# Optimization experiments

Hardware: AMD Instinct MI355X
Metric: run time of the kernel (lower is better)

The kernel has to match this reference:

```python
import jax, jax.numpy as jnp
import numpy as np

C_S = 384; C_Z = 128; C_RES = 128; H = 12; HD = 32; L = 8; RB = 2; NA = 7
TSF = 10.0; EPS = 1e-8; B = 2; N = 512; NRES = 21


def layernorm(x, g, b, eps=1e-5):
    m = jnp.mean(x, -1, keepdims=True)
    v = jnp.mean((x - m) ** 2, -1, keepdims=True)
    return (x - m) * jax.lax.rsqrt(v + eps) * g + b


def lin(x, w, b=None):
    y = x @ w.T
    return y if b is None else y + b


def rot_vec(R, v):
    return jnp.einsum('...ij,...j->...i', R, v)


def make_rigid(n, ca, c, eps=1e-7):
    # Gram-Schmidt backbone frame construction (openfold make_transform_from_reference)
    t = -ca
    n_xyz = n + t; c_xyz = c + t
    cx, cy, cz = c_xyz[..., 0], c_xyz[..., 1], c_xyz[..., 2]
    z = jnp.zeros_like(cx); o = jnp.ones_like(cx)
    nrm = jnp.sqrt(eps + cx**2 + cy**2)
    s1 = -cy / nrm; c1 = cx / nrm
    R1 = jnp.stack([jnp.stack([c1, -s1, z], -1), jnp.stack([s1, c1, z], -1), jnp.stack([z, z, o], -1)], -2)
    nrm2 = jnp.sqrt(eps + cx**2 + cy**2 + cz**2)
    s2 = cz / nrm2; c2 = jnp.sqrt(cx**2 + cy**2) / nrm2
    R2 = jnp.stack([jnp.stack([c2, z, s2], -1), jnp.stack([z, o, z], -1), jnp.stack([-s2, z, c2], -1)], -2)
    Rc = R2 @ R1
    n2 = rot_vec(Rc, n_xyz)
    ny, nz = n2[..., 1], n2[..., 2]
    nrm3 = jnp.sqrt(eps + ny**2 + nz**2)
    sn = -nz / nrm3; cn = ny / nrm3
    Rn = jnp.stack([jnp.stack([o, z, z], -1), jnp.stack([z, cn, -sn], -1), jnp.stack([z, sn, cn], -1)], -2)
    R = jnp.swapaxes(Rn @ Rc, -1, -2)
    return R, ca


def to4x4(R, t):
    bot = jnp.zeros(R.shape[:-2] + (1, 4), R.dtype).at[..., 0, 3].set(1.0)
    top = jnp.concatenate([R, t[..., None]], -1)
    return jnp.concatenate([top, bot], -2)


def compose(R1, t1, R2, t2):
    return R1 @ R2, rot_vec(R1, t2) + t1


def structure_fwd(s, z, aatype, mask, ln_s_g, ln_s_b, ln_z_g, ln_z_b, w_in, b_in, w_b, b_b,
                  attn_ln_g, attn_ln_b, attn_wqkv, attn_wo, attn_bo, attn_wg, attn_bg,
                  tr_ln_g, tr_ln_b, tr_w1, tr_b1, tr_w2, tr_b2, w_bb, b_bb,
                  ar_win, ar_bin, ar_winit, ar_binit, ar_w1, ar_b1, ar_w2, ar_b2, ar_wout, ar_bout,
                  default_frames, group_idx, atom_mask, lit_positions):
    Bd, Nd = s.shape[:2]
    s = layernorm(s, ln_s_g, ln_s_b)
    s_init = s
    s = lin(s, w_in, b_in)
    zn = layernorm(z, ln_z_g, ln_z_b)
    bmat = lin(zn, w_b, b_b)                                # [B,N,N,L*H]
    bmat = jnp.transpose(bmat, (0, 3, 1, 2)).reshape(Bd, L, H, Nd, Nd)
    key_mask = (mask[:, None, None, :] == 0)
    for i in range(L):
        xn = layernorm(s, attn_ln_g[i], attn_ln_b[i])
        t = lin(xn, attn_wqkv[i]).reshape(Bd, Nd, H, 3 * HD).transpose(0, 2, 1, 3)
        q, k, v = jnp.split(t, 3, axis=-1)                  # each [B,H,N,HD]
        a = jnp.einsum('bhqc,bhkc->bhqk', q * HD ** -0.5, k) + bmat[:, i]
        a = jnp.where(key_mask, -1e9, a)
        a = jax.nn.softmax(a, axis=-1)
        y = jnp.einsum('bhqk,bhkc->bqhc', a, v).reshape(Bd, Nd, C_S)
        g = jax.nn.sigmoid(lin(xn, attn_wg[i], attn_bg[i]))
        s = s + lin(g * y, attn_wo[i], attn_bo[i])
        xt = layernorm(s, tr_ln_g[i], tr_ln_b[i])
        s = s + lin(jax.nn.relu(lin(xt, tr_w1[i], tr_b1[i])), tr_w2[i], tr_b2[i])
    # angle resnet
    a0 = lin(jax.nn.relu(s_init), ar_winit, ar_binit)
    a = lin(jax.nn.relu(s), ar_win, ar_bin) + a0
    for j in range(RB):
        h = lin(jax.nn.relu(a), ar_w1[j], ar_b1[j])
        h = lin(jax.nn.relu(h), ar_w2[j], ar_b2[j])
        a = a + h
    ang = lin(jax.nn.relu(a), ar_wout, ar_bout).reshape(Bd, Nd, NA, 2)
    unnorm = ang
    denom = jnp.sqrt(jnp.maximum(jnp.sum(ang ** 2, -1, keepdims=True), EPS))
    angles = ang / denom
    # backbone rigid from predicted pseudo-atoms
    n_, ca_, c_ = jnp.split(lin(s, w_bb, b_bb), 3, axis=-1)
    Rbb, tbb = make_rigid(n_, ca_, c_)
    tbb = tbb * TSF
    # torsion_angles_to_frames
    d4 = default_frames[aatype]                             # [B,N,8,4,4]
    dR = d4[..., :3, :3]; dt = d4[..., :3, 3]
    bb_sin = jnp.zeros(angles.shape[:-2] + (1,), angles.dtype)
    bb_cos = jnp.ones_like(bb_sin)
    sin_a = jnp.concatenate([bb_sin, angles[..., 0]], -1)   # [B,N,8]
    cos_a = jnp.concatenate([bb_cos, angles[..., 1]], -1)
    z8 = jnp.zeros_like(sin_a); o8 = jnp.ones_like(sin_a)
    Ra = jnp.stack([jnp.stack([o8, z8, z8], -1), jnp.stack([z8, cos_a, -sin_a], -1), jnp.stack([z8, sin_a, cos_a], -1)], -2)
    Rf = dR @ Ra; tf = dt
    R5, t5 = compose(Rf[..., 4, :, :], tf[..., 4, :], Rf[..., 5, :, :], tf[..., 5, :])
    R6, t6 = compose(R5, t5, Rf[..., 6, :, :], tf[..., 6, :])
    R7, t7 = compose(R6, t6, Rf[..., 7, :, :], tf[..., 7, :])
    Rall = jnp.concatenate([Rf[..., :5, :, :], jnp.stack([R5, R6, R7], -3)], -3)
    tall = jnp.concatenate([tf[..., :5, :], jnp.stack([t5, t6, t7], -2)], -2)
    Rg = jnp.einsum('bnij,bngjk->bngik', Rbb, Rall)
    tg = jnp.einsum('bnij,bngj->bngi', Rbb, tall) + tbb[..., None, :]
    # frames + literature positions -> atom14
    oh = jax.nn.one_hot(group_idx[aatype], 8, dtype=Rg.dtype)   # [B,N,14,8]
    Ratom = jnp.einsum('bnag,bngij->bnaij', oh, Rg)
    tatom = jnp.einsum('bnag,bngi->bnai', oh, tg)
    lit = lit_positions[aatype]                             # [B,N,14,3]
    pred = jnp.einsum('bnaij,bnaj->bnai', Ratom, lit) + tatom
    pred = pred * atom_mask[aatype][..., None]
    return angles, unnorm, to4x4(Rbb, tbb), to4x4(Rg, tg), pred, s


def setup_inputs():
    key = jax.random.key(0)
    ks = iter(jax.random.split(key, 64))
    nrm = lambda shape: jax.random.normal(next(ks), shape, jnp.float32) * 0.02
    d = {}
    d['s'] = jax.random.normal(next(ks), (B, N, C_S), jnp.float32)
    d['z'] = jax.random.normal(next(ks), (B, N, N, C_Z), jnp.float32)
    d['aatype'] = jax.random.randint(next(ks), (B, N), 0, NRES)
    d['mask'] = jax.random.randint(next(ks), (B, N), 0, 2).astype(jnp.int32)
    d['ln_s_g'] = jnp.ones(C_S); d['ln_s_b'] = jnp.zeros(C_S)
    d['ln_z_g'] = jnp.ones(C_Z); d['ln_z_b'] = jnp.zeros(C_Z)
    d['w_in'] = nrm((C_S, C_S)); d['b_in'] = jnp.zeros(C_S)
    d['w_b'] = nrm((L * H, C_Z)); d['b_b'] = jnp.zeros(L * H)
    d['attn_ln_g'] = jnp.ones((L, C_S)); d['attn_ln_b'] = jnp.zeros((L, C_S))
    d['attn_wqkv'] = nrm((L, 3 * C_S, C_S))
    d['attn_wo'] = nrm((L, C_S, C_S)); d['attn_bo'] = jnp.zeros((L, C_S))
    d['attn_wg'] = nrm((L, C_S, C_S)); d['attn_bg'] = jnp.ones((L, C_S))
    d['tr_ln_g'] = jnp.ones((L, C_S)); d['tr_ln_b'] = jnp.zeros((L, C_S))
    d['tr_w1'] = nrm((L, C_S, C_S)); d['tr_b1'] = jnp.zeros((L, C_S))
    d['tr_w2'] = nrm((L, C_S, C_S)); d['tr_b2'] = jnp.zeros((L, C_S))
    d['w_bb'] = nrm((9, C_S)); d['b_bb'] = jnp.zeros(9)
    d['ar_win'] = nrm((C_RES, C_S)); d['ar_bin'] = jnp.zeros(C_RES)
    d['ar_winit'] = nrm((C_RES, C_S)); d['ar_binit'] = jnp.zeros(C_RES)
    d['ar_w1'] = nrm((RB, C_RES, C_RES)); d['ar_b1'] = jnp.zeros((RB, C_RES))
    d['ar_w2'] = nrm((RB, C_RES, C_RES)); d['ar_b2'] = jnp.zeros((RB, C_RES))
    d['ar_wout'] = nrm((2 * NA, C_RES)); d['ar_bout'] = jnp.zeros(2 * NA)
    df = jnp.tile(jnp.eye(4, dtype=jnp.float32), (NRES, 8, 1, 1))
    df = df.at[..., :3, 3].set(jax.random.normal(next(ks), (NRES, 8, 3)))
    d['default_frames'] = df
    d['group_idx'] = jax.random.randint(next(ks), (NRES, 14), 0, 8)
    d['atom_mask'] = (jax.random.uniform(next(ks), (NRES, 14)) < 0.9).astype(jnp.float32)
    d['lit_positions'] = jax.random.normal(next(ks), (NRES, 14, 3), jnp.float32)
    return d


def reference(s, z, aatype, mask, ln_s_g, ln_s_b, ln_z_g, ln_z_b, w_in, b_in, w_b, b_b,
              attn_ln_g, attn_ln_b, attn_wqkv, attn_wo, attn_bo, attn_wg, attn_bg,
              tr_ln_g, tr_ln_b, tr_w1, tr_b1, tr_w2, tr_b2, w_bb, b_bb,
              ar_win, ar_bin, ar_winit, ar_binit, ar_w1, ar_b1, ar_w2, ar_b2, ar_wout, ar_bout,
              default_frames, group_idx, atom_mask, lit_positions):
    return structure_fwd(s, z, aatype, mask, ln_s_g, ln_s_b, ln_z_g, ln_z_b, w_in, b_in, w_b, b_b,
                         attn_ln_g, attn_ln_b, attn_wqkv, attn_wo, attn_bo, attn_wg, attn_bg,
                         tr_ln_g, tr_ln_b, tr_w1, tr_b1, tr_w2, tr_b2, w_bb, b_bb,
                         ar_win, ar_bin, ar_winit, ar_binit, ar_w1, ar_b1, ar_w2, ar_b2, ar_wout, ar_bout,
                         default_frames, group_idx, atom_mask, lit_positions)
```

## Files before the change

### kernel.cpp

```cpp
#include <hip/hip_runtime.h>
#include <hip/hip_bf16.h>

typedef __attribute__((ext_vector_type(8))) short bf16x8;
typedef __attribute__((ext_vector_type(4))) float f32x4;
typedef unsigned short u16;

__device__ __forceinline__ u16 f2bf(float f) {
  union { __hip_bfloat16 b; u16 u; } v;
  v.b = __float2bfloat16(f);
  return v.u;
}
__device__ __forceinline__ float bf2f(u16 s) {
  union { unsigned u; float f; } v; v.u = ((unsigned)s) << 16;
  return v.f;
}
__device__ __forceinline__ f32x4 mfma_bf16(bf16x8 a, bf16x8 b, f32x4 c) {
  return __builtin_amdgcn_mfma_f32_16x16x32_bf16(a, b, c, 0, 0, 0);
}
__device__ __forceinline__ void split2(float x, u16& h, u16& l) {
  h = f2bf(x);
  l = f2bf(x - bf2f(h));
}
template <int SPL>
__device__ __forceinline__ void splitN(float x, u16* o) {
// ... 30 lines not shown
}
struct P3 { const float* s; u16* d; int n; };
struct Prep3Args { P3 j[4]; };
__global__ __launch_bounds__(256) void prep3_kernel(Prep3Args A, int total4) {
  for (int i4 = blockIdx.x * 256 + threadIdx.x; i4 < total4; i4 += gridDim.x * 256) {
    int i = i4 * 4;
    #pragma unroll
    for (int jj = 0; jj < 4; jj++) {
      if (i < A.j[jj].n) {
        const float* src = A.j[jj].s;
        u16* d0 = A.j[jj].d;
        u16* d1 = d0 + A.j[jj].n;
        u16* d2 = d1 + A.j[jj].n;
        float4 v = *(const float4*)(src + i);
        float xv[4] = {v.x, v.y, v.z, v.w};
        ushort4 o0, o1, o2;
        u16* po0 = (u16*)&o0; u16* po1 = (u16*)&o1; u16* po2 = (u16*)&o2;
        #pragma unroll
        for (int e = 0; e < 4; e++) {
          u16 tmp[3]; splitN<3>(xv[e], tmp);
          po0[e] = tmp[0]; po1[e] = tmp[1]; po2[e] = tmp[2];
        }
        *(ushort4*)(d0 + i) = o0;
        *(ushort4*)(d1 + i) = o1;
        *(ushort4*)(d2 + i) = o2;
        break;
      }
      i -= A.j[jj].n;
    }
  }
}

__global__ __launch_bounds__(256) void ln_kernel(
    const float* __restrict__ x, const float* __restrict__ gamma,
    const float* __restrict__ beta, float* __restrict__ o, int rows, int C) {
  int wid = threadIdx.x >> 6, lane = threadIdx.x & 63;
  int row = blockIdx.x * 4 + wid;
  if (row >= rows) return;
  const float* xr = x + (size_t)row * C;
  float s = 0.f, s2 = 0.f;
  for (int c = lane; c < C; c += 64) { float v = xr[c]; s += v; s2 += v * v; }
  #pragma unroll
  for (int off = 32; off >= 1; off >>= 1) {
    s += __shfl_xor(s, off);
    s2 += __shfl_xor(s2, off);
  }
  float m = s / C;
  float var = s2 / C - m * m;
  float rs = rsqrtf(var + 1e-5f);
  float* orow = o + (size_t)row * C;
  for (int c = lane; c < C; c += 64) orow[c] = (xr[c] - m) * rs * gamma[c] + beta[c];
}

template <int SPL, int LNA, int INRELU, int ACT, int ACC, int STATS, int OUT2>
__global__ __launch_bounds__(128) void gemm_kernel(
    const float* __restrict__ A, const float* __restrict__ pin,
    const float* __restrict__ lng, const float* __restrict__ lnb,
    const u16* __restrict__ w0p, const u16* __restrict__ w1p, const u16* __restrict__ w2p,
    const float* __restrict__ bias,
    float* __restrict__ O, float* __restrict__ O2, float* __restrict__ pout,
    int M, int N, int K) {
  __shared__ __align__(16) u16 a_pl[SPL][16][72];
  __shared__ __align__(16) u16 w_pl[SPL][64][72];
  const int n0 = blockIdx.x * 64, m0 = blockIdx.y * 16;
  const int t = threadIdx.x;
  const int wid = t >> 6, lane = t & 63;
  const int cl = lane & 15, cg = lane >> 4;
  const int ar = t >> 3, aq = t & 7;
  const int wr = t >> 1, wh2 = t & 1;
  const float* ap = A + (size_t)(m0 + ar) * K + aq * 8;
  const u16* wp[3] = {nullptr, nullptr, nullptr};
  {
    const u16* tmp[3] = {w0p, w1p, w2p};
    #pragma unroll
    for (int p = 0; p < SPL; p++) wp[p] = tmp[p] + (size_t)(n0 + wr) * K + wh2 * 32;
  }
  float rm = 0.f, rrs = 1.f;
  if (LNA) {
    float s = 0.f, s2 = 0.f;
    #pragma unroll
    for (int pq = 0; pq < 12; pq++) {
      s  += pin[(m0 + ar) * 32 + pq * 2];
      s2 += pin[(m0 + ar) * 32 + pq * 2 + 1];
    }
    rm = s * (1.f / 384.f);
    rrs = rsqrtf(s2 * (1.f / 384.f) - rm * rm + 1e-5f);
  }
  float4 ra[2], rg[2], rb4[2];
  uint4 rw[SPL][4];
  auto GLOAD = [&](int k0) {
    ra[0] = ((const float4*)(ap + k0))[0];
    ra[1] = ((const float4*)(ap + k0))[1];
    #pragma unroll
    for (int p = 0; p < SPL; p++)
      #pragma unroll
      for (int e = 0; e < 4; e++) rw[p][e] = *(const uint4*)(wp[p] + k0 + e * 8);
    if (LNA) {
      rg[0]  = ((const float4*)(lng + k0 + aq * 8))[0];
      rg[1]  = ((const float4*)(lng + k0 + aq * 8))[1];
      rb4[0] = ((const float4*)(lnb + k0 + aq * 8))[0];
      rb4[1] = ((const float4*)(lnb + k0 + aq * 8))[1];
    }
  };
  GLOAD(0);
  f32x4 acc[2] = {};
  for (int k0 = 0; k0 < K; k0 += 64) {
    {
      float av[8] = {ra[0].x, ra[0].y, ra[0].z, ra[0].w, ra[1].x, ra[1].y, ra[1].z, ra[1].w};
      if (LNA) {
        float gv[8] = {rg[0].x, rg[0].y, rg[0].z, rg[0].w, rg[1].x, rg[1].y, rg[1].z, rg[1].w};
        float bv[8] = {rb4[0].x, rb4[0].y, rb4[0].z, rb4[0].w, rb4[1].x, rb4[1].y, rb4[1].z, rb4[1].w};
        #pragma unroll
        for (int j = 0; j < 8; j++) av[j] = (av[j] - rm) * rrs * gv[j] + bv[j];
      }
      if (INRELU) {
        #pragma unroll
        for (int j = 0; j < 8; j++) av[j] = fmaxf(av[j], 0.f);
      }
      u16 sh[SPL][8];
      #pragma unroll
      for (int j = 0; j < 8; j++) {
        u16 tmp[SPL]; splitN<SPL>(av[j], tmp);
        #pragma unroll
        for (int p = 0; p < SPL; p++) sh[p][j] = tmp[p];
      }
      #pragma unroll
      for (int p = 0; p < SPL; p++) {
        *(uint4*)&a_pl[p][ar][aq * 8] = *(const uint4*)&sh[p][0];
        #pragma unroll
        for (int e = 0; e < 4; e++) *(uint4*)&w_pl[p][wr][wh2 * 32 + e * 8] = rw[p][e];
      }
    }
    __syncthreads();
    if (k0 + 64 < K) GLOAD(k0 + 64);
    #pragma unroll
    for (int ks2 = 0; ks2 < 2; ks2++) {
      bf16x8 av_[SPL];
      #pragma unroll
      for (int p = 0; p < SPL; p++)
        av_[p] = *(const bf16x8*)&a_pl[p][cl][ks2 * 32 + cg * 8];
      bf16x8 bv[SPL][2];
      #pragma unroll
      for (int p = 0; p < SPL; p++)
        #pragma unroll
        for (int ntl = 0; ntl < 2; ntl++)
          bv[p][ntl] = *(const bf16x8*)&w_pl[p][(wid * 2 + ntl) * 16 + cl][ks2 * 32 + cg * 8];
      #pragma unroll
      for (int d = 0; d < SPL; d++)
        #pragma unroll
        for (int i2 = 0; i2 <= d; i2++) {
          #pragma unroll
          for (int ntl = 0; ntl < 2; ntl++)
            acc[ntl] = mfma_bf16(av_[i2], bv[d - i2][ntl], acc[ntl]);
        }
    }
    __syncthreads();
  }
  float ps[4], ps2[4];
  #pragma unroll
  for (int i = 0; i < 4; i++) { ps[i] = 0.f; ps2[i] = 0.f; }
  #pragma unroll
  for (int ntl = 0; ntl < 2; ntl++) {
    #pragma unroll
    for (int i = 0; i < 4; i++) {
      int r = m0 + cg * 4 + i;
      int c = n0 + (wid * 2 + ntl) * 16 + cl;
      float v = acc[ntl][i];
      if (bias) v += bias[c];
      if (ACT == 1) v = fmaxf(v, 0.f);
      if (ACT == 2) v = 1.f / (1.f + __expf(-v));
      size_t oi = (size_t)r * N + c;
      float nv = ACC ? (O[oi] + v) : v;
      O[oi] = nv;
      if (OUT2) O2[oi] = nv;
      if (STATS) { ps[i] += nv; ps2[i] += nv * nv; }
    }
  }
  if (STATS) {
    #pragma unroll
    for (int i = 0; i < 4; i++) {
      #pragma unroll
      for (int off = 1; off < 16; off <<= 1) {
        ps[i] += __shfl_xor(ps[i], off);
        ps2[i] += __shfl_xor(ps2[i], off);
      }
    }
    if (cl == 0) {
      #pragma unroll
      for (int i = 0; i < 4; i++) {
        int r = m0 + cg * 4 + i;
        pout[r * 32 + (blockIdx.x * 2 + wid) * 2] = ps[i];
        pout[r * 32 + (blockIdx.x * 2 + wid) * 2 + 1] = ps2[i];
      }
    }
  }
}

__global__ __launch_bounds__(128) void gemm_qkvg_kernel(
    const float* __restrict__ A, const float* __restrict__ pin,
    const float* __restrict__ lng, const float* __restrict__ lnb,
    const u16* __restrict__ wqh, const u16* __restrict__ wql,
    const u16* __restrict__ wgh, const u16* __restrict__ wgl,
    const float* __restrict__ bg,
    u16* __restrict__ qkvh, u16* __restrict__ qkvl, float* __restrict__ gbuf) {
  __shared__ __align__(16) u16 a_pl[2][16][72];
  __shared__ __align__(16) u16 w_pl[2][64][72];
  const int n0 = blockIdx.x * 64, m0 = blockIdx.y * 16;
  const bool isg = (n0 >= 1152);
  const int t = threadIdx.x;
  const int wid = t >> 6, lane = t & 63;
  const int cl = lane & 15, cg = lane >> 4;
  const int ar = t >> 3, aq = t & 7;
  const int wr = t >> 1, wh2 = t & 1;
  const float* ap = A + (size_t)(m0 + ar) * 384 + aq * 8;
  const u16* wph = (isg ? wgh + (size_t)(n0 - 1152 + wr) * 384 : wqh + (size_t)(n0 + wr) * 384) + wh2 * 32;
  const u16* wpl = (isg ? wgl + (size_t)(n0 - 1152 + wr) * 384 : wql + (size_t)(n0 + wr) * 384) + wh2 * 32;
  float s = 0.f, s2 = 0.f;
  #pragma unroll
  for (int pq = 0; pq < 12; pq++) {
    s  += pin[(m0 + ar) * 32 + pq * 2];
    s2 += pin[(m0 + ar) * 32 + pq * 2 + 1];
  }
  const float rm = s * (1.f / 384.f);
  const float rrs = rsqrtf(s2 * (1.f / 384.f) - rm * rm + 1e-5f);
  float4 ra[2], rg[2], rb4[2];
  uint4 rwh[4], rwl[4];
  auto GLOAD = [&](int k0) {
    ra[0] = ((const float4*)(ap + k0))[0];
    ra[1] = ((const float4*)(ap + k0))[1];
    #pragma unroll
    for (int e = 0; e < 4; e++) {
      rwh[e] = *(const uint4*)(wph + k0 + e * 8);
      rwl[e] = *(const uint4*)(wpl + k0 + e * 8);
    }
    rg[0]  = ((const float4*)(lng + k0 + aq * 8))[0];
    rg[1]  = ((const float4*)(lng + k0 + aq * 8))[1];
    rb4[0] = ((const float4*)(lnb + k0 + aq * 8))[0];
    rb4[1] = ((const float4*)(lnb + k0 + aq * 8))[1];
  };
  GLOAD(0);
  f32x4 acc[2] = {};
  for (int k0 = 0; k0 < 384; k0 += 64) {
    {
      float av[8] = {ra[0].x, ra[0].y, ra[0].z, ra[0].w, ra[1].x, ra[1].y, ra[1].z, ra[1].w};
      float gv[8] = {rg[0].x, rg[0].y, rg[0].z, rg[0].w, rg[1].x, rg[1].y, rg[1].z, rg[1].w};
      float bv[8] = {rb4[0].x, rb4[0].y, rb4[0].z, rb4[0].w, rb4[1].x, rb4[1].y, rb4[1].z, rb4[1].w};
      u16 sh[2][8];
      #pragma unroll
      for (int j = 0; j < 8; j++) {
        float x = (av[j] - rm) * rrs * gv[j] + bv[j];
        split2(x, sh[0][j], sh[1][j]);
      }
      #pragma unroll
      for (int p = 0; p < 2; p++) *(uint4*)&a_pl[p][ar][aq * 8] = *(const uint4*)&sh[p][0];
      #pragma unroll
      for (int e = 0; e < 4; e++) {
        *(uint4*)&w_pl[0][wr][wh2 * 32 + e * 8] = rwh[e];
        *(uint4*)&w_pl[1][wr][wh2 * 32 + e * 8] = rwl[e];
      }
    }
    __syncthreads();
    if (k0 + 64 < 384) GLOAD(k0 + 64);
    #pragma unroll
    for (int ks2 = 0; ks2 < 2; ks2++) {
      bf16x8 ah = *(const bf16x8*)&a_pl[0][cl][ks2 * 32 + cg * 8];
      bf16x8 al = *(const bf16x8*)&a_pl[1][cl][ks2 * 32 + cg * 8];
      bf16x8 bh[2], bl[2];
      #pragma unroll
      for (int ntl = 0; ntl < 2; ntl++) {
        bh[ntl] = *(const bf16x8*)&w_pl[0][(wid * 2 + ntl) * 16 + cl][ks2 * 32 + cg * 8];
        bl[ntl] = *(const bf16x8*)&w_pl[1][(wid * 2 + ntl) * 16 + cl][ks2 * 32 + cg * 8];
      }
      #pragma unroll
      for (int ntl = 0; ntl < 2; ntl++) {
        acc[ntl] = mfma_bf16(ah, bh[ntl], acc[ntl]);
        acc[ntl] = mfma_bf16(ah, bl[ntl], acc[ntl]);
        acc[ntl] = mfma_bf16(al, bh[ntl], acc[ntl]);
      }
    }
    __syncthreads();
  }
  #pragma unroll
  for (int ntl = 0; ntl < 2; ntl++) {
    #pragma unroll
    for (int i = 0; i < 4; i++) {
      int r = m0 + cg * 4 + i;
      int c = n0 + (wid * 2 + ntl) * 16 + cl;
      float v = acc[ntl][i];
      if (isg) {
        int cc = c - 1152;
        v = 1.f / (1.f + __expf(-(v + bg[cc])));
        gbuf[(size_t)r * 384 + cc] = v;
      } else {
        u16 hh, ll; split2(v, hh, ll);
        qkvh[(size_t)r * 1152 + c] = hh;
        qkvl[(size_t)r * 1152 + c] = ll;
      }
    }
  }
}

__global__ __launch_bounds__(512) void zbmat_kernel(
    const float* __restrict__ z, const float* __restrict__ gamma,
    const float* __restrict__ beta, const u16* __restrict__ wbh,
    const u16* __restrict__ wbl, const float* __restrict__ bbias,
    float* __restrict__ bm) {
  __shared__ __align__(16) u16 w_h[96][136], w_l[96][136];
  __shared__ __align__(16) u16 a_h[2][64][136], a_l[2][64][136];
  const int b = blockIdx.x >> 9, i = blockIdx.x & 511;
  const int t = threadIdx.x;
  for (int idx = t; idx < 1536; idx += 512) {
    int r2 = idx >> 4, c2 = (idx & 15) * 8;
    *(uint4*)&w_h[r2][c2] = *(const uint4*)(wbh + r2 * 128 + c2);
    *(uint4*)&w_l[r2][c2] = *(const uint4*)(wbl + r2 * 128 + c2);
  }
  const int r = t >> 3, q = t & 7;
  const int cq = q * 16;
  const float* zbase = z + ((size_t)(b * 512 + i) * 512) * 128 + (size_t)r * 128 + cq;
  float4 gv[4], bv[4];
  #pragma unroll
  for (int ii = 0; ii < 4; ii++) {
    gv[ii] = *(const float4*)(gamma + cq + ii * 4);
    bv[ii] = *(const float4*)(beta + cq + ii * 4);
  }
  const int wid = t >> 6, lane = t & 63;
  const int cl = lane & 15, cg = lane >> 4;
  const int m = wid & 3, g = wid >> 2;
  const int arow = m * 16 + cl;
  float bb[3];
  #pragma unroll
  for (int nt = 0; nt < 3; nt++) bb[nt] = bbias[(g * 3 + nt) * 16 + cl];
  float4 v[4];

  auto ln_store = [&](int dst) {
    float s = 0.f, s2 = 0.f;
    #pragma unroll
    for (int ii = 0; ii < 4; ii++) {
      s += v[ii].x + v[ii].y + v[ii].z + v[ii].w;
      s2 += v[ii].x * v[ii].x + v[ii].y * v[ii].y + v[ii].z * v[ii].z + v[ii].w * v[ii].w;
    }
    s += __shfl_xor(s, 1); s2 += __shfl_xor(s2, 1);
    s += __shfl_xor(s, 2); s2 += __shfl_xor(s2, 2);
    s += __shfl_xor(s, 4); s2 += __shfl_xor(s2, 4);
    const float mu = s * (1.f / 128.f);
    const float var = s2 * (1.f / 128.f) - mu * mu;
    const float rs = rsqrtf(var + 1e-5f);
    float xv[16];
    #pragma unroll
    for (int w2 = 0; w2 < 4; w2++) {
      float4 x = v[w2], g2 = gv[w2], be = bv[w2];
// ... 375 lines not shown
  const float* lit_pos   = (const float*)d_in[40];

  char* p = (char*)d_ws;
  float* bmat   = (float*)p;          p += 201326592;
  float* s_init = (float*)p;          p += 1572864;
  float* s_cur  = (float*)p;          p += 1572864;
  u16*   qkvh   = (u16*)p;            p += 2359296;
  u16*   qkvl   = (u16*)p;            p += 2359296;
  float* gbuf   = (float*)p;          p += 1572864;
  float* ybuf   = (float*)p;          p += 1572864;
  float* h1buf  = (float*)p;          p += 1572864;
  float* abuf   = (float*)p;          p += 524288;
  float* htmp   = (float*)p;          p += 524288;
  float* pbuf   = (float*)p;          p += 131072;
  float* bbbuf  = (float*)p;          p += 65536;
  float* angraw = (float*)p;          p += 57344;
  u16* ps_qkvw  = (u16*)p;            p += 14155776;
  u16* ps_wg    = (u16*)p;            p += 4718592;
  u16* ps_wo    = (u16*)p;            p += 4718592;
  u16* ps_tr1   = (u16*)p;            p += 4718592;
  u16* ps_tr2   = (u16*)p;            p += 4718592;
  u16* ps_win   = (u16*)p;            p += 589824;
  u16* ps_wb    = (u16*)p;            p += 49152;
  u16* ps_arwin = (u16*)p;            p += 294912;
  u16* ps_arwinit = (u16*)p;          p += 294912;
  u16* ps_arw1  = (u16*)p;            p += 196608;
  u16* ps_arw2  = (u16*)p;            p += 196608;

  float* out    = (float*)d_out;
  float* o_ang  = out;
  float* o_un   = out + 14336;
  float* o_bb4  = out + 28672;
  float* o_rg4  = out + 45056;
  float* o_pred = out + 176128;
  float* o_s    = out + 219136;

  Prep2Args p2;
  p2.j[0] = {attn_wqkv, ps_qkvw, 3538944};
  p2.j[1] = {attn_wg,   ps_wg,   1179648};
  p2.j[2] = {attn_wo,   ps_wo,   1179648};
  p2.j[3] = {tr_w1,     ps_tr1,  1179648};
  p2.j[4] = {tr_w2,     ps_tr2,  1179648};
  p2.j[5] = {w_in,      ps_win,  147456};
  p2.j[6] = {w_b,       ps_wb,   12288};
  prep2_kernel<<<2048, 256, 0, stream>>>(p2, 2104320);
  Prep3Args p3;
  p3.j[0] = {ar_win,   ps_arwin,   49152};
  p3.j[1] = {ar_winit, ps_arwinit, 49152};
  p3.j[2] = {ar_w1,    ps_arw1,    32768};
  p3.j[3] = {ar_w2,    ps_arw2,    32768};
  prep3_kernel<<<160, 256, 0, stream>>>(p3, 40960);

  ln_kernel<<<256, 256, 0, stream>>>(s_in, ln_s_g, ln_s_b, s_init, 1024, 384);
  gemm_kernel<2, 0, 0, 0, 0, 1, 0><<<dim3(6, 64), 128, 0, stream>>>(
      s_init, nullptr, nullptr, nullptr, ps_win, ps_win + 147456, nullptr,
      b_in, s_cur, nullptr, pbuf, 1024, 384, 384);
  zbmat_kernel<<<1024, 512, 0, stream>>>(z_in, ln_z_g, ln_z_b, ps_wb, ps_wb + 12288, b_b, bmat);

  for (int l = 0; l < 8; ++l) {
    gemm_qkvg_kernel<<<dim3(24, 64), 128, 0, stream>>>(
        s_cur, pbuf, attn_ln_g + l * 384, attn_ln_b + l * 384,
        ps_qkvw + (size_t)l * 442368, ps_qkvw + 3538944 + (size_t)l * 442368,
        ps_wg + (size_t)l * 147456, ps_wg + 1179648 + (size_t)l * 147456,
        attn_bg + l * 384, qkvh, qkvl, gbuf);
    attn_kernel<<<384, 128, 0, stream>>>(qkvh, qkvl, bmat, maskp, gbuf, ybuf, l);
    gemm_kernel<2, 0, 0, 0, 1, 1, 0><<<dim3(6, 64), 128, 0, stream>>>(
        ybuf, nullptr, nullptr, nullptr,
        ps_wo + (size_t)l * 147456, ps_wo + 1179648 + (size_t)l * 147456, nullptr,
        attn_bo + l * 384, s_cur, nullptr, pbuf, 1024, 384, 384);
    gemm_kernel<2, 1, 0, 1, 0, 0, 0><<<dim3(6, 64), 128, 0, stream>>>(
        s_cur, pbuf, tr_ln_g + l * 384, tr_ln_b + l * 384,
        ps_tr1 + (size_t)l * 147456, ps_tr1 + 1179648 + (size_t)l * 147456, nullptr,
        tr_b1 + l * 384, h1buf, nullptr, nullptr, 1024, 384, 384);
    if (l < 7)
      gemm_kernel<2, 0, 0, 0, 1, 1, 0><<<dim3(6, 64), 128, 0, stream>>>(
          h1buf, nullptr, nullptr, nullptr,
          ps_tr2 + (size_t)l * 147456, ps_tr2 + 1179648 + (size_t)l * 147456, nullptr,
          tr_b2 + l * 384, s_cur, nullptr, pbuf, 1024, 384, 384);
    else
      gemm_kernel<2, 0, 0, 0, 1, 1, 1><<<dim3(6, 64), 128, 0, stream>>>(
          h1buf, nullptr, nullptr, nullptr,
          ps_tr2 + (size_t)l * 147456, ps_tr2 + 1179648 + (size_t)l * 147456, nullptr,
          tr_b2 + l * 384, s_cur, o_s, pbuf, 1024, 384, 384);
  }

  gemm_kernel<3, 0, 1, 0, 0, 0, 0><<<dim3(2, 64), 128, 0, stream>>>(
      s_cur, nullptr, nullptr, nullptr,
      ps_arwin, ps_arwin + 49152, ps_arwin + 98304,
      ar_bin, abuf, nullptr, nullptr, 1024, 128, 384);
  gemm_kernel<3, 0, 1, 0, 1, 0, 0><<<dim3(2, 64), 128, 0, stream>>>(
      s_init, nullptr, nullptr, nullptr,
      ps_arwinit, ps_arwinit + 49152, ps_arwinit + 98304,
      ar_binit, abuf, nullptr, nullptr, 1024, 128, 384);
  for (int j = 0; j < 2; ++j) {
    gemm_kernel<3, 0, 1, 0, 0, 0, 0><<<dim3(2, 64), 128, 0, stream>>>(
        abuf, nullptr, nullptr, nullptr,
        ps_arw1 + j * 16384, ps_arw1 + 32768 + j * 16384, ps_arw1 + 65536 + j * 16384,
        ar_b1 + j * 128, htmp, nullptr, nullptr, 1024, 128, 128);
    gemm_kernel<3, 0, 1, 0, 1, 0, 0><<<dim3(2, 64), 128, 0, stream>>>(
        htmp, nullptr, nullptr, nullptr,
        ps_arw2 + j * 16384, ps_arw2 + 32768 + j * 16384, ps_arw2 + 65536 + j * 16384,
        ar_b2 + j * 128, abuf, nullptr, nullptr, 1024, 128, 128);
  }

  proj_kernel<9, 384, 0><<<256, 256, 0, stream>>>(s_cur, w_bb, b_bb, bbbuf);
  proj_kernel<14, 128, 1><<<256, 256, 0, stream>>>(abuf, ar_wout, ar_bout, angraw);
  tail_kernel<<<4, 256, 0, stream>>>(angraw, bbbuf, aatype, def_frames, group_idx,
                                     atom_mask, lit_pos, o_ang, o_un, o_bb4, o_rg4, o_pred);
}
```

Before: 1.369 ms.

## Keep full-K weight tiles resident in LDS across multiple M tiles in GEMMs

The 384-wide GEMMs now load the whole 64x384 hi/lo weight slab and the LayerNorm gamma/beta into LDS once per block. Each block then loops over several 16-row M tiles, prefetching the next A rows while it computes, so weights are reused instead of reloaded by many small blocks. The angle-resnet GEMMs move to a 32-row tile variant so each weight load serves twice as many rows. The cost is much larger LDS use per block (about 130KB), which lowers occupancy, and far fewer blocks in the grid.

```diff
diff --git a/kernel.cpp b/kernel.cpp
--- a/kernel.cpp
+++ b/kernel.cpp
@@ -106,250 +106,336 @@
   for (int c = lane; c < C; c += 64) orow[c] = (xr[c] - m) * rs * gamma[c] + beta[c];
 }
 
-template <int SPL, int LNA, int INRELU, int ACT, int ACC, int STATS, int OUT2>
-__global__ __launch_bounds__(128) void gemm_kernel(
+template <int LNA, int ACT, int ACC, int STATS, int OUT2>
+__global__ __launch_bounds__(128) void gemm_ml_kernel(
     const float* __restrict__ A, const float* __restrict__ pin,
     const float* __restrict__ lng, const float* __restrict__ lnb,
-    const u16* __restrict__ w0p, const u16* __restrict__ w1p, const u16* __restrict__ w2p,
+    const u16* __restrict__ wh_, const u16* __restrict__ wl_,
     const float* __restrict__ bias,
     float* __restrict__ O, float* __restrict__ O2, float* __restrict__ pout,
-    int M, int N, int K) {
-  __shared__ __align__(16) u16 a_pl[SPL][16][72];
-  __shared__ __align__(16) u16 w_pl[SPL][64][72];
-  const int n0 = blockIdx.x * 64, m0 = blockIdx.y * 16;
+    int N, int MT) {
+  __shared__ __align__(16) u16 w_pl[2][64][392];
+  __shared__ __align__(16) u16 a_pl[2][16][392];
+  __shared__ float gbs[2][384];
+  const int n0 = blockIdx.x * 64;
+  const int m0g = blockIdx.y * (MT << 4);
   const int t = threadIdx.x;
   const int wid = t >> 6, lane = t & 63;
   const int cl = lane & 15, cg = lane >> 4;
-  const int ar = t >> 3, aq = t & 7;
-  const int wr = t >> 1, wh2 = t & 1;
-  const float* ap = A + (size_t)(m0 + ar) * K + aq * 8;
-  const u16* wp[3] = {nullptr, nullptr, nullptr};
   {
-    const u16* tmp[3] = {w0p, w1p, w2p};
-    #pragma unroll
-    for (int p = 0; p < SPL; p++) wp[p] = tmp[p] + (size_t)(n0 + wr) * K + wh2 * 32;
-  }
-  float rm = 0.f, rrs = 1.f;
-  if (LNA) {
-    float s = 0.f, s2 = 0.f;
-    #pragma unroll
-    for (int pq = 0; pq < 12; pq++) {
-      s  += pin[(m0 + ar) * 32 + pq * 2];
-      s2 += pin[(m0 + ar) * 32 + pq * 2 + 1];
-    }
-    rm = s * (1.f / 384.f);
-    rrs = rsqrtf(s2 * (1.f / 384.f) - rm * rm + 1e-5f);
-  }
-  float4 ra[2], rg[2], rb4[2];
-  uint4 rw[SPL][4];
-  auto GLOAD = [&](int k0) {
-    ra[0] = ((const float4*)(ap + k0))[0];
-    ra[1] = ((const float4*)(ap + k0))[1];
-    #pragma unroll
-    for (int p = 0; p < SPL; p++)
-      #pragma unroll
-      for (int e = 0; e < 4; e++) rw[p][e] = *(const uint4*)(wp[p] + k0 + e * 8);
+    const u16* s0 = wh_ + (size_t)n0 * 384;
+    const u16* s1 = wl_ + (size_t)n0 * 384;
+    for (int idx = t; idx < 3072; idx += 128) {
+      int r = idx / 48, c8 = (idx % 48) * 8;
+      *(uint4*)&w_pl[0][r][c8] = *(const uint4*)(s0 + (size_t)r * 384 + c8);
+      *(uint4*)&w_pl[1][r][c8] = *(const uint4*)(s1 + (size_t)r * 384 + c8);
+    }
     if (LNA) {
-      rg[0]  = ((const float4*)(lng + k0 + aq * 8))[0];
-      rg[1]  = ((const float4*)(lng + k0 + aq * 8))[1];
-      rb4[0] = ((const float4*)(lnb + k0 + aq * 8))[0];
-      rb4[1] = ((const float4*)(lnb + k0 + aq * 8))[1];
-    }
-  };
-  GLOAD(0);
-  f32x4 acc[2] = {};
-  for (int k0 = 0; k0 < K; k0 += 64) {
-    {
-      float av[8] = {ra[0].x, ra[0].y, ra[0].z, ra[0].w, ra[1].x, ra[1].y, ra[1].z, ra[1].w};
-      if (LNA) {
-        float gv[8] = {rg[0].x, rg[0].y, rg[0].z, rg[0].w, rg[1].x, rg[1].y, rg[1].z, rg[1].w};
-        float bv[8] = {rb4[0].x, rb4[0].y, rb4[0].z, rb4[0].w, rb4[1].x, rb4[1].y, rb4[1].z, rb4[1].w};
+      for (int idx = t; idx < 384; idx += 128) {
+        gbs[0][idx] = lng[idx];
+        gbs[1][idx] = lnb[idx];
+      }
+    }
+  }
+  const int arow = t >> 3;
+  const int alane = t & 7;
+  const float* abase = A + (size_t)(m0g + arow) * 384 + alane * 4;
+  float4 ra[12];
+  #pragma unroll
+  for (int e = 0; e < 12; e++) ra[e] = *(const float4*)(abase + e * 32);
+  __syncthreads();
+  for (int mt = 0; mt < MT; mt++) {
+    const int rowa = m0g + mt * 16 + arow;
+    float rm = 0.f, rrs = 1.f;
+    if (LNA) {
+      float s = 0.f, s2 = 0.f;
+      #pragma unroll
+      for (int pq = 0; pq < 12; pq++) {
+        s  += pin[rowa * 32 + pq * 2];
+        s2 += pin[rowa * 32 + pq * 2 + 1];
+      }
+      rm = s * (1.f / 384.f);
+      rrs = rsqrtf(s2 * (1.f / 384.f) - rm * rm + 1e-5f);
+    }
+    #pragma unroll
+    for (int e = 0; e < 12; e++) {
+      int col = e * 32 + alane * 4;
+      float xv[4] = {ra[e].x, ra[e].y, ra[e].z, ra[e].w};
+      ushort4 h4, l4;
+      u16* ph = (u16*)&h4; u16* pl = (u16*)&l4;
+      #pragma unroll
+      for (int j = 0; j < 4; j++) {
+        float x = xv[j];
+        if (LNA) x = (x - rm) * rrs * gbs[0][col + j] + gbs[1][col + j];
+        split2(x, ph[j], pl[j]);
+      }
+      *(ushort4*)&a_pl[0][arow][col] = h4;
+      *(ushort4*)&a_pl[1][arow][col] = l4;
+    }
+    __syncthreads();
+    if (mt + 1 < MT) {
+      const float* src = abase + (size_t)(mt + 1) * 16 * 384;
+      #pragma unroll
+      for (int e = 0; e < 12; e++) ra[e] = *(const float4*)(src + e * 32);
+    }
+    f32x4 acc[2] = {};
+    #pragma unroll
+    for (int ks = 0; ks < 12; ks++) {
+      bf16x8 ah = *(const bf16x8*)&a_pl[0][cl][ks * 32 + cg * 8];
+      bf16x8 al = *(const bf16x8*)&a_pl[1][cl][ks * 32 + cg * 8];
+      bf16x8 bh0 = *(const bf16x8*)&w_pl[0][(wid * 2 + 0) * 16 + cl][ks * 32 + cg * 8];
+      bf16x8 bh1 = *(const bf16x8*)&w_pl[0][(wid * 2 + 1) * 16 + cl][ks * 32 + cg * 8];
+      bf16x8 bl0 = *(const bf16x8*)&w_pl[1][(wid * 2 + 0) * 16 + cl][ks * 32 + cg * 8];
+      bf16x8 bl1 = *(const bf16x8*)&w_pl[1][(wid * 2 + 1) * 16 + cl][ks * 32 + cg * 8];
+      acc[0] = mfma_bf16(ah, bh0, acc[0]);
+      acc[1] = mfma_bf16(ah, bh1, acc[1]);
+      acc[0] = mfma_bf16(ah, bl0, acc[0]);
+      acc[1] = mfma_bf16(ah, bl1, acc[1]);
+      acc[0] = mfma_bf16(al, bh0, acc[0]);
+      acc[1] = mfma_bf16(al, bh1, acc[1]);
+    }
+    float ps[4], ps2[4];
+    #pragma unroll
+    for (int i = 0; i < 4; i++) { ps[i] = 0.f; ps2[i] = 0.f; }
+    #pragma unroll
+    for (int ntl = 0; ntl < 2; ntl++) {
+      #pragma unroll
+      for (int i = 0; i < 4; i++) {
+        int r = m0g + mt * 16 + cg * 4 + i;
+        int c = n0 + (wid * 2 + ntl) * 16 + cl;
+        float v = acc[ntl][i];
+        if (bias) v += bias[c];
+        if (ACT == 1) v = fmaxf(v, 0.f);
+        size_t oi = (size_t)r * N + c;
+        float nv = ACC ? (O[oi] + v) : v;
+        O[oi] = nv;
+        if (OUT2) O2[oi] = nv;
+        if (STATS) { ps[i] += nv; ps2[i] += nv * nv; }
+      }
+    }
+    if (STATS) {
+      #pragma unroll
+      for (int i = 0; i < 4; i++) {
         #pragma unroll
-        for (int j = 0; j < 8; j++) av[j] = (av[j] - rm) * rrs * gv[j] + bv[j];
-      }
-      if (INRELU) {
+        for (int off = 1; off < 16; off <<= 1) {
+          ps[i] += __shfl_xor(ps[i], off);
+          ps2[i] += __shfl_xor(ps2[i], off);
+        }
+      }
+      if (cl == 0) {
         #pragma unroll
-        for (int j = 0; j < 8; j++) av[j] = fmaxf(av[j], 0.f);
-      }
-      u16 sh[SPL][8];
-      #pragma unroll
-      for (int j = 0; j < 8; j++) {
-        u16 tmp[SPL]; splitN<SPL>(av[j], tmp);
-        #pragma unroll
-        for (int p = 0; p < SPL; p++) sh[p][j] = tmp[p];
-      }
-      #pragma unroll
-      for (int p = 0; p < SPL; p++) {
-        *(uint4*)&a_pl[p][ar][aq * 8] = *(const uint4*)&sh[p][0];
-        #pragma unroll
-        for (int e = 0; e < 4; e++) *(uint4*)&w_pl[p][wr][wh2 * 32 + e * 8] = rw[p][e];
+        for (int i = 0; i < 4; i++) {
+          int r = m0g + mt * 16 + cg * 4 + i;
+          pout[r * 32 + (blockIdx.x * 2 + wid) * 2] = ps[i];
+          pout[r * 32 + (blockIdx.x * 2 + wid) * 2 + 1] = ps2[i];
+        }
       }
     }
     __syncthreads();
-    if (k0 + 64 < K) GLOAD(k0 + 64);
-    #pragma unroll
-    for (int ks2 = 0; ks2 < 2; ks2++) {
-      bf16x8 av_[SPL];
-      #pragma unroll
-      for (int p = 0; p < SPL; p++)
-        av_[p] = *(const bf16x8*)&a_pl[p][cl][ks2 * 32 + cg * 8];
-      bf16x8 bv[SPL][2];
-      #pragma unroll
-      for (int p = 0; p < SPL; p++)
-        #pragma unroll
-        for (int ntl = 0; ntl < 2; ntl++)
-          bv[p][ntl] = *(const bf16x8*)&w_pl[p][(wid * 2 + ntl) * 16 + cl][ks2 * 32 + cg * 8];
-      #pragma unroll
-      for (int d = 0; d < SPL; d++)
-        #pragma unroll
-        for (int i2 = 0; i2 <= d; i2++) {
-          #pragma unroll
-          for (int ntl = 0; ntl < 2; ntl++)
-            acc[ntl] = mfma_bf16(av_[i2], bv[d - i2][ntl], acc[ntl]);
-        }
-    }
-    __syncthreads();
-  }
-  float ps[4], ps2[4];
-  #pragma unroll
-  for (int i = 0; i < 4; i++) { ps[i] = 0.f; ps2[i] = 0.f; }
-  #pragma unroll
-  for (int ntl = 0; ntl < 2; ntl++) {
-    #pragma unroll
-    for (int i = 0; i < 4; i++) {
-      int r = m0 + cg * 4 + i;
-      int c = n0 + (wid * 2 + ntl) * 16 + cl;
-      float v = acc[ntl][i];
-      if (bias) v += bias[c];
-      if (ACT == 1) v = fmaxf(v, 0.f);
-      if (ACT == 2) v = 1.f / (1.f + __expf(-v));
-      size_t oi = (size_t)r * N + c;
-      float nv = ACC ? (O[oi] + v) : v;
-      O[oi] = nv;
-      if (OUT2) O2[oi] = nv;
-      if (STATS) { ps[i] += nv; ps2[i] += nv * nv; }
-    }
-  }
-  if (STATS) {
-    #pragma unroll
-    for (int i = 0; i < 4; i++) {
-      #pragma unroll
-      for (int off = 1; off < 16; off <<= 1) {
-        ps[i] += __shfl_xor(ps[i], off);
-        ps2[i] += __shfl_xor(ps2[i], off);
-      }
-    }
-    if (cl == 0) {
-      #pragma unroll
-      for (int i = 0; i < 4; i++) {
-        int r = m0 + cg * 4 + i;
-        pout[r * 32 + (blockIdx.x * 2 + wid) * 2] = ps[i];
-        pout[r * 32 + (blockIdx.x * 2 + wid) * 2 + 1] = ps2[i];
-      }
-    }
-  }
-}
-
-__global__ __launch_bounds__(128) void gemm_qkvg_kernel(
+  }
+}
+
+__global__ __launch_bounds__(128) void gemm_qkvg_ml_kernel(
     const float* __restrict__ A, const float* __restrict__ pin,
     const float* __restrict__ lng, const float* __restrict__ lnb,
     const u16* __restrict__ wqh, const u16* __restrict__ wql,
     const u16* __restrict__ wgh, const u16* __restrict__ wgl,
     const float* __restrict__ bg,
-    u16* __restrict__ qkvh, u16* __restrict__ qkvl, float* __restrict__ gbuf) {
-  __shared__ __align__(16) u16 a_pl[2][16][72];
-  __shared__ __align__(16) u16 w_pl[2][64][72];
-  const int n0 = blockIdx.x * 64, m0 = blockIdx.y * 16;
+    u16* __restrict__ qkvh, u16* __restrict__ qkvl, float* __restrict__ gbuf,
+    int MT) {
+  __shared__ __align__(16) u16 w_pl[2][64][392];
+  __shared__ __align__(16) u16 a_pl[2][16][392];
+  __shared__ float gbs[2][384];
+  const int n0 = blockIdx.x * 64;
   const bool isg = (n0 >= 1152);
+  const int m0g = blockIdx.y * (MT << 4);
   const int t = threadIdx.x;
   const int wid = t >> 6, lane = t & 63;
   const int cl = lane & 15, cg = lane >> 4;
-  const int ar = t >> 3, aq = t & 7;
+  {
+    const u16* s0 = isg ? wgh + (size_t)(n0 - 1152) * 384 : wqh + (size_t)n0 * 384;
+    const u16* s1 = isg ? wgl + (size_t)(n0 - 1152) * 384 : wql + (size_t)n0 * 384;
+    for (int idx = t; idx < 3072; idx += 128) {
+      int r = idx / 48, c8 = (idx % 48) * 8;
+      *(uint4*)&w_pl[0][r][c8] = *(const uint4*)(s0 + (size_t)r * 384 + c8);
+      *(uint4*)&w_pl[1][r][c8] = *(const uint4*)(s1 + (size_t)r * 384 + c8);
+    }
+    for (int idx = t; idx < 384; idx += 128) {
+      gbs[0][idx] = lng[idx];
+      gbs[1][idx] = lnb[idx];
+    }
+  }
+  const int arow = t >> 3;
+  const int alane = t & 7;
+  const float* abase = A + (size_t)(m0g + arow) * 384 + alane * 4;
+  float4 ra[12];
+  #pragma unroll
+  for (int e = 0; e < 12; e++) ra[e] = *(const float4*)(abase + e * 32);
+  __syncthreads();
+  for (int mt = 0; mt < MT; mt++) {
+    const int rowa = m0g + mt * 16 + arow;
+    float s = 0.f, s2 = 0.f;
+    #pragma unroll
+    for (int pq = 0; pq < 12; pq++) {
+      s  += pin[rowa * 32 + pq * 2];
+      s2 += pin[rowa * 32 + pq * 2 + 1];
+    }
+    const float rm = s * (1.f / 384.f);
+    const float rrs = rsqrtf(s2 * (1.f / 384.f) - rm * rm + 1e-5f);
+    #pragma unroll
+    for (int e = 0; e < 12; e++) {
+      int col = e * 32 + alane * 4;
+      float xv[4] = {ra[e].x, ra[e].y, ra[e].z, ra[e].w};
+      ushort4 h4, l4;
+      u16* ph = (u16*)&h4; u16* pl = (u16*)&l4;
+      #pragma unroll
+      for (int j = 0; j < 4; j++) {
+        float x = (xv[j] - rm) * rrs * gbs[0][col + j] + gbs[1][col + j];
+        split2(x, ph[j], pl[j]);
+      }
+      *(ushort4*)&a_pl[0][arow][col] = h4;
+      *(ushort4*)&a_pl[1][arow][col] = l4;
+    }
+    __syncthreads();
+    if (mt + 1 < MT) {
+      const float* src = abase + (size_t)(mt + 1) * 16 * 384;
+      #pragma unroll
+      for (int e = 0; e < 12; e++) ra[e] = *(const float4*)(src + e * 32);
+    }
+    f32x4 acc[2] = {};
+    #pragma unroll
+    for (int ks = 0; ks < 12; ks++) {
+      bf16x8 ah = *(const bf16x8*)&a_pl[0][cl][ks * 32 + cg * 8];
+      bf16x8 al = *(const bf16x8*)&a_pl[1][cl][ks * 32 + cg * 8];
+      bf16x8 bh0 = *(const bf16x8*)&w_pl[0][(wid * 2 + 0) * 16 + cl][ks * 32 + cg * 8];
+      bf16x8 bh1 = *(const bf16x8*)&w_pl[0][(wid * 2 + 1) * 16 + cl][ks * 32 + cg * 8];
+      bf16x8 bl0 = *(const bf16x8*)&w_pl[1][(wid * 2 + 0) * 16 + cl][ks * 32 + cg * 8];
+      bf16x8 bl1 = *(const bf16x8*)&w_pl[1][(wid * 2 + 1) * 16 + cl][ks * 32 + cg * 8];
+      acc[0] = mfma_bf16(ah, bh0, acc[0]);
+      acc[1] = mfma_bf16(ah, bh1, acc[1]);
+      acc[0] = mfma_bf16(ah, bl0, acc[0]);
+      acc[1] = mfma_bf16(ah, bl1, acc[1]);
+      acc[0] = mfma_bf16(al, bh0, acc[0]);
+      acc[1] = mfma_bf16(al, bh1, acc[1]);
+    }
+    #pragma unroll
+    for (int ntl = 0; ntl < 2; ntl++) {
+      #pragma unroll
+      for (int i = 0; i < 4; i++) {
+        int r = m0g + mt * 16 + cg * 4 + i;
+        int c = n0 + (wid * 2 + ntl) * 16 + cl;
+        float v = acc[ntl][i];
+        if (isg) {
+          int cc = c - 1152;
+          v = 1.f / (1.f + __expf(-(v + bg[cc])));
+          gbuf[(size_t)r * 384 + cc] = v;
+        } else {
+          u16 hh, ll; split2(v, hh, ll);
+          qkvh[(size_t)r * 1152 + c] = hh;
+          qkvl[(size_t)r * 1152 + c] = ll;
+        }
+      }
+    }
+    __syncthreads();
+  }
+}
+
+template <int SPL, int INRELU, int ACT, int ACC>
+__global__ __launch_bounds__(128) void gemm32_kernel(
+    const float* __restrict__ A,
+    const u16* __restrict__ w0p, const u16* __restrict__ w1p, const u16* __restrict__ w2p,
+    const float* __restrict__ bias,
+    float* __restrict__ O, int M, int N, int K) {
+  __shared__ __align__(16) u16 a_pl[SPL][32][72];
+  __shared__ __align__(16) u16 w_pl[SPL][64][72];
+  const int n0 = blockIdx.x * 64, m0 = blockIdx.y * 32;
+  const int t = threadIdx.x;
+  const int wid = t >> 6, lane = t & 63;
+  const int cl = lane & 15, cg = lane >> 4;
+  const int ar = t >> 2, aq = t & 3;
   const int wr = t >> 1, wh2 = t & 1;
-  const float* ap = A + (size_t)(m0 + ar) * 384 + aq * 8;
-  const u16* wph = (isg ? wgh + (size_t)(n0 - 1152 + wr) * 384 : wqh + (size_t)(n0 + wr) * 384) + wh2 * 32;
-  const u16* wpl = (isg ? wgl + (size_t)(n0 - 1152 + wr) * 384 : wql + (size_t)(n0 + wr) * 384) + wh2 * 32;
-  float s = 0.f, s2 = 0.f;
-  #pragma unroll
-  for (int pq = 0; pq < 12; pq++) {
-    s  += pin[(m0 + ar) * 32 + pq * 2];
-    s2 += pin[(m0 + ar) * 32 + pq * 2 + 1];
-  }
-  const float rm = s * (1.f / 384.f);
-  const float rrs = rsqrtf(s2 * (1.f / 384.f) - rm * rm + 1e-5f);
-  float4 ra[2], rg[2], rb4[2];
-  uint4 rwh[4], rwl[4];
+  const float* ap = A + (size_t)(m0 + ar) * K + aq * 16;
+  const u16* wp[3] = {nullptr, nullptr, nullptr};
+  {
+    const u16* tmp[3] = {w0p, w1p, w2p};
+    #pragma unroll
+    for (int p = 0; p < SPL; p++) wp[p] = tmp[p] + (size_t)(n0 + wr) * K + wh2 * 32;
+  }
+  float4 ra[4];
+  uint4 rw[SPL][4];
   auto GLOAD = [&](int k0) {
-    ra[0] = ((const float4*)(ap + k0))[0];
-    ra[1] = ((const float4*)(ap + k0))[1];
-    #pragma unroll
-    for (int e = 0; e < 4; e++) {
-      rwh[e] = *(const uint4*)(wph + k0 + e * 8);
-      rwl[e] = *(const uint4*)(wpl + k0 + e * 8);
-    }
-    rg[0]  = ((const float4*)(lng + k0 + aq * 8))[0];
-    rg[1]  = ((const float4*)(lng + k0 + aq * 8))[1];
-    rb4[0] = ((const float4*)(lnb + k0 + aq * 8))[0];
-    rb4[1] = ((const float4*)(lnb + k0 + aq * 8))[1];
+    #pragma unroll
+    for (int e = 0; e < 4; e++) ra[e] = ((const float4*)(ap + k0))[e];
+    #pragma unroll
+    for (int p = 0; p < SPL; p++)
+      #pragma unroll
+      for (int e = 0; e < 4; e++) rw[p][e] = *(const uint4*)(wp[p] + k0 + e * 8);
   };
   GLOAD(0);
-  f32x4 acc[2] = {};
-  for (int k0 = 0; k0 < 384; k0 += 64) {
+  f32x4 acc[4] = {};
+  for (int k0 = 0; k0 < K; k0 += 64) {
     {
-      float av[8] = {ra[0].x, ra[0].y, ra[0].z, ra[0].w, ra[1].x, ra[1].y, ra[1].z, ra[1].w};
-      float gv[8] = {rg[0].x, rg[0].y, rg[0].z, rg[0].w, rg[1].x, rg[1].y, rg[1].z, rg[1].w};
-      float bv[8] = {rb4[0].x, rb4[0].y, rb4[0].z, rb4[0].w, rb4[1].x, rb4[1].y, rb4[1].z, rb4[1].w};
-      u16 sh[2][8];
-      #pragma unroll
-      for (int j = 0; j < 8; j++) {
-        float x = (av[j] - rm) * rrs * gv[j] + bv[j];
-        split2(x, sh[0][j], sh[1][j]);
-      }
-      #pragma unroll
-      for (int p = 0; p < 2; p++) *(uint4*)&a_pl[p][ar][aq * 8] = *(const uint4*)&sh[p][0];
+      float av[16];
       #pragma unroll
       for (int e = 0; e < 4; e++) {
-        *(uint4*)&w_pl[0][wr][wh2 * 32 + e * 8] = rwh[e];
-        *(uint4*)&w_pl[1][wr][wh2 * 32 + e * 8] = rwl[e];
+        av[e * 4 + 0] = ra[e].x; av[e * 4 + 1] = ra[e].y;
+        av[e * 4 + 2] = ra[e].z; av[e * 4 + 3] = ra[e].w;
+      }
+      if (INRELU) {
+        #pragma unroll
+        for (int j = 0; j < 16; j++) av[j] = fmaxf(av[j], 0.f);
+      }
+      u16 sh[SPL][16];
+      #pragma unroll
+      for (int j = 0; j < 16; j++) {
+        u16 tmp[SPL]; splitN<SPL>(av[j], tmp);
+        #pragma unroll
+        for (int p = 0; p < SPL; p++) sh[p][j] = tmp[p];
+      }
+      #pragma unroll
+      for (int p = 0; p < SPL; p++) {
+        *(uint4*)&a_pl[p][ar][aq * 16]     = *(const uint4*)&sh[p][0];
+        *(uint4*)&a_pl[p][ar][aq * 16 + 8] = *(const uint4*)&sh[p][8];
+        #pragma unroll
+        for (int e = 0; e < 4; e++) *(uint4*)&w_pl[p][wr][wh2 * 32 + e * 8] = rw[p][e];
       }
     }
     __syncthreads();
-    if (k0 + 64 < 384) GLOAD(k0 + 64);
+    if (k0 + 64 < K) GLOAD(k0 + 64);
     #pragma unroll
     for (int ks2 = 0; ks2 < 2; ks2++) {
-      bf16x8 ah = *(const bf16x8*)&a_pl[0][cl][ks2 * 32 + cg * 8];
-      bf16x8 al = *(const bf16x8*)&a_pl[1][cl][ks2 * 32 + cg * 8];
-      bf16x8 bh[2], bl[2];
-      #pragma unroll
-      for (int ntl = 0; ntl < 2; ntl++) {
-        bh[ntl] = *(const bf16x8*)&w_pl[0][(wid * 2 + ntl) * 16 + cl][ks2 * 32 + cg * 8];
-        bl[ntl] = *(const bf16x8*)&w_pl[1][(wid * 2 + ntl) * 16 + cl][ks2 * 32 + cg * 8];
-      }
-      #pragma unroll
-      for (int ntl = 0; ntl < 2; ntl++) {
-        acc[ntl] = mfma_bf16(ah, bh[ntl], acc[ntl]);
-        acc[ntl] = mfma_bf16(ah, bl[ntl], acc[ntl]);
-        acc[ntl] = mfma_bf16(al, bh[ntl], acc[ntl]);
-      }
+      bf16x8 av_[SPL];
+      #pragma unroll
+      for (int p = 0; p < SPL; p++)
+        av_[p] = *(const bf16x8*)&a_pl[p][wid * 16 + cl][ks2 * 32 + cg * 8];
+      bf16x8 bv[SPL][4];
+      #pragma unroll
+      for (int p = 0; p < SPL; p++)
+        #pragma unroll
+        for (int nt = 0; nt < 4; nt++)
+          bv[p][nt] = *(const bf16x8*)&w_pl[p][nt * 16 + cl][ks2 * 32 + cg * 8];
+      #pragma unroll
+      for (int d = 0; d < SPL; d++)
+        #pragma unroll
+        for (int i2 = 0; i2 <= d; i2++) {
+          #pragma unroll
+          for (int nt = 0; nt < 4; nt++)
+            acc[nt] = mfma_bf16(av_[i2], bv[d - i2][nt], acc[nt]);
+        }
     }
     __syncthreads();
   }
   #pragma unroll
-  for (int ntl = 0; ntl < 2; ntl++) {
+  for (int nt = 0; nt < 4; nt++) {
     #pragma unroll
     for (int i = 0; i < 4; i++) {
-      int r = m0 + cg * 4 + i;
-      int c = n0 + (wid * 2 + ntl) * 16 + cl;
-      float v = acc[ntl][i];
-      if (isg) {
-        int cc = c - 1152;
-        v = 1.f / (1.f + __expf(-(v + bg[cc])));
-        gbuf[(size_t)r * 384 + cc] = v;
-      } else {
-        u16 hh, ll; split2(v, hh, ll);
-        qkvh[(size_t)r * 1152 + c] = hh;
-        qkvl[(size_t)r * 1152 + c] = ll;
-      }
+      int r = m0 + wid * 16 + cg * 4 + i;
+      int c = n0 + nt * 16 + cl;
+      float v = acc[nt][i];
+      if (bias) v += bias[c];
+      if (ACT == 1) v = fmaxf(v, 0.f);
+      size_t oi = (size_t)r * N + c;
+      if (ACC) O[oi] += v; else O[oi] = v;
     }
   }
 }
@@ -831,55 +917,51 @@
   prep3_kernel<<<160, 256, 0, stream>>>(p3, 40960);
 
   ln_kernel<<<256, 256, 0, stream>>>(s_in, ln_s_g, ln_s_b, s_init, 1024, 384);
-  gemm_kernel<2, 0, 0, 0, 0, 1, 0><<<dim3(6, 64), 128, 0, stream>>>(
-      s_init, nullptr, nullptr, nullptr, ps_win, ps_win + 147456, nullptr,
-      b_in, s_cur, nullptr, pbuf, 1024, 384, 384);
+  gemm_ml_kernel<0, 0, 0, 1, 0><<<dim3(6, 16), 128, 0, stream>>>(
+      s_init, nullptr, nullptr, nullptr, ps_win, ps_win + 147456,
+      b_in, s_cur, nullptr, pbuf, 384, 4);
   zbmat_kernel<<<1024, 512, 0, stream>>>(z_in, ln_z_g, ln_z_b, ps_wb, ps_wb + 12288, b_b, bmat);
 
   for (int l = 0; l < 8; ++l) {
-    gemm_qkvg_kernel<<<dim3(24, 64), 128, 0, stream>>>(
+    gemm_qkvg_ml_kernel<<<dim3(24, 8), 128, 0, stream>>>(
         s_cur, pbuf, attn_ln_g + l * 384, attn_ln_b + l * 384,
         ps_qkvw + (size_t)l * 442368, ps_qkvw + 3538944 + (size_t)l * 442368,
         ps_wg + (size_t)l * 147456, ps_wg + 1179648 + (size_t)l * 147456,
-        attn_bg + l * 384, qkvh, qkvl, gbuf);
+        attn_bg + l * 384, qkvh, qkvl, gbuf, 8);
     attn_kernel<<<384, 128, 0, stream>>>(qkvh, qkvl, bmat, maskp, gbuf, ybuf, l);
-    gemm_kernel<2, 0, 0, 0, 1, 1, 0><<<dim3(6, 64), 128, 0, stream>>>(
+    gemm_ml_kernel<0, 0, 1, 1, 0><<<dim3(6, 16), 128, 0, stream>>>(
         ybuf, nullptr, nullptr, nullptr,
-        ps_wo + (size_t)l * 147456, ps_wo + 1179648 + (size_t)l * 147456, nullptr,
-        attn_bo + l * 384, s_cur, nullptr, pbuf, 1024, 384, 384);
-    gemm_kernel<2, 1, 0, 1, 0, 0, 0><<<dim3(6, 64), 128, 0, stream>>>(
+        ps_wo + (size_t)l * 147456, ps_wo + 1179648 + (size_t)l * 147456,
+        attn_bo + l * 384, s_cur, nullptr, pbuf, 384, 4);
+    gemm_ml_kernel<1, 1, 0, 0, 0><<<dim3(6, 16), 128, 0, stream>>>(
         s_cur, pbuf, tr_ln_g + l * 384, tr_ln_b + l * 384,
-        ps_tr1 + (size_t)l * 147456, ps_tr1 + 1179648 + (size_t)l * 147456, nullptr,
-        tr_b1 + l * 384, h1buf, nullptr, nullptr, 1024, 384, 384);
+        ps_tr1 + (size_t)l * 147456, ps_tr1 + 1179648 + (size_t)l * 147456,
+        tr_b1 + l * 384, h1buf, nullptr, nullptr, 384, 4);
     if (l < 7)
-      gemm_kernel<2, 0, 0, 0, 1, 1, 0><<<dim3(6, 64), 128, 0, stream>>>(
+      gemm_ml_kernel<0, 0, 1, 1, 0><<<dim3(6, 16), 128, 0, stream>>>(
           h1buf, nullptr, nullptr, nullptr,
-          ps_tr2 + (size_t)l * 147456, ps_tr2 + 1179648 + (size_t)l * 147456, nullptr,
-          tr_b2 + l * 384, s_cur, nullptr, pbuf, 1024, 384, 384);
+          ps_tr2 + (size_t)l * 147456, ps_tr2 + 1179648 + (size_t)l * 147456,
+          tr_b2 + l * 384, s_cur, nullptr, pbuf, 384, 4);
     else
-      gemm_kernel<2, 0, 0, 0, 1, 1, 1><<<dim3(6, 64), 128, 0, stream>>>(
+      gemm_ml_kernel<0, 0, 1, 1, 1><<<dim3(6, 16), 128, 0, stream>>>(
           h1buf, nullptr, nullptr, nullptr,
-          ps_tr2 + (size_t)l * 147456, ps_tr2 + 1179648 + (size_t)l * 147456, nullptr,
-          tr_b2 + l * 384, s_cur, o_s, pbuf, 1024, 384, 384);
-  }
-
-  gemm_kernel<3, 0, 1, 0, 0, 0, 0><<<dim3(2, 64), 128, 0, stream>>>(
-      s_cur, nullptr, nullptr, nullptr,
-      ps_arwin, ps_arwin + 49152, ps_arwin + 98304,
-      ar_bin, abuf, nullptr, nullptr, 1024, 128, 384);
-  gemm_kernel<3, 0, 1, 0, 1, 0, 0><<<dim3(2, 64), 128, 0, stream>>>(
-      s_init, nullptr, nullptr, nullptr,
-      ps_arwinit, ps_arwinit + 49152, ps_arwinit + 98304,
-      ar_binit, abuf, nullptr, nullptr, 1024, 128, 384);
+          ps_tr2 + (size_t)l * 147456, ps_tr2 + 1179648 + (size_t)l * 147456,
+          tr_b2 + l * 384, s_cur, o_s, pbuf, 384, 4);
+  }
+
+  gemm32_kernel<3, 1, 0, 0><<<dim3(2, 32), 128, 0, stream>>>(
+      s_cur, ps_arwin, ps_arwin + 49152, ps_arwin + 98304,
+      ar_bin, abuf, 1024, 128, 384);
+  gemm32_kernel<3, 1, 0, 1><<<dim3(2, 32), 128, 0, stream>>>(
+      s_init, ps_arwinit, ps_arwinit + 49152, ps_arwinit + 98304,
+      ar_binit, abuf, 1024, 128, 384);
   for (int j = 0; j < 2; ++j) {
-    gemm_kernel<3, 0, 1, 0, 0, 0, 0><<<dim3(2, 64), 128, 0, stream>>>(
-        abuf, nullptr, nullptr, nullptr,
-        ps_arw1 + j * 16384, ps_arw1 + 32768 + j * 16384, ps_arw1 + 65536 + j * 16384,
-        ar_b1 + j * 128, htmp, nullptr, nullptr, 1024, 128, 128);
-    gemm_kernel<3, 0, 1, 0, 1, 0, 0><<<dim3(2, 64), 128, 0, stream>>>(
-        htmp, nullptr, nullptr, nullptr,
-        ps_arw2 + j * 16384, ps_arw2 + 32768 + j * 16384, ps_arw2 + 65536 + j * 16384,
-        ar_b2 + j * 128, abuf, nullptr, nullptr, 1024, 128, 128);
+    gemm32_kernel<3, 1, 0, 0><<<dim3(2, 32), 128, 0, stream>>>(
+        abuf, ps_arw1 + j * 16384, ps_arw1 + 32768 + j * 16384, ps_arw1 + 65536 + j * 16384,
+        ar_b1 + j * 128, htmp, 1024, 128, 128);
+    gemm32_kernel<3, 1, 0, 1><<<dim3(2, 32), 128, 0, stream>>>(
+        htmp, ps_arw2 + j * 16384, ps_arw2 + 32768 + j * 16384, ps_arw2 + 65536 + j * 16384,
+        ar_b2 + j * 128, abuf, 1024, 128, 128);
   }
 
   proj_kernel<9, 384, 0><<<256, 256, 0, stream>>>(s_cur, w_bb, b_bb, bbbuf);
```

New measurement: 1.556 ms. 1.14x slower.
